# Kernel tuning notes

Hardware: AMD Instinct MI355X
Metric: run time of the kernel (lower is better)

The kernel has to match this reference:

```python
import jax, jax.numpy as jnp
import numpy as np

B, M, V, E, IN, OUT = 65536, 1_000_000, 2_000_000, 1_310_720, 64, 32
ALPHA = 0.2  # LeakyReLU negative slope (pyGAT default)


def setup_inputs() -> dict:
    key = jax.random.key(0)
    ks = jax.random.split(key, 11)
    return {
        "emb": jax.random.normal(ks[0], (V, IN), jnp.float32) * 0.1,
        "W_bal": jax.random.normal(ks[1], (IN, OUT), jnp.float32) * 0.1,
        "a_bal": jax.random.normal(ks[2], (2 * OUT,), jnp.float32) * 0.1,
        "W_unbal": jax.random.normal(ks[3], (IN, OUT), jnp.float32) * 0.1,
        "a_unbal": jax.random.normal(ks[4], (2 * OUT,), jnp.float32) * 0.1,
        "unique_ids": jax.random.randint(ks[5], (M,), 0, V, jnp.int32),
        "self_cols": jax.random.randint(ks[6], (B,), 0, M, jnp.int32),
        "pos_rows": jax.random.randint(ks[7], (E,), 0, B, jnp.int32),
        "pos_cols": jax.random.randint(ks[8], (E,), 0, M, jnp.int32),
        "neg_rows": jax.random.randint(ks[9], (E,), 0, B, jnp.int32),
        "neg_cols": jax.random.randint(ks[10], (E,), 0, M, jnp.int32),
    }


def _sp_gat(x, W, a, rows, cols, n_rows):
    # x: [M, IN] unique-node embeddings; rows: [Etot] in [0, n_rows); cols: [Etot] in [0, M)
    h = x @ W                                   # [M, OUT]
    src = h[rows]                               # [Etot, OUT] row-side features
    dst = h[cols]                               # [Etot, OUT] neighbor features
    score = jax.nn.leaky_relu(src @ a[:OUT] + dst @ a[OUT:], negative_slope=ALPHA)
    e = jnp.exp(-score)                         # [Etot] unnormalized attention
    denom = jax.ops.segment_sum(e, rows, num_segments=n_rows)            # [n_rows]
    num = jax.ops.segment_sum(e[:, None] * dst, rows, num_segments=n_rows)  # [n_rows, OUT]
    return jax.nn.elu(num / denom[:, None])


def reference(emb, W_bal, a_bal, W_unbal, a_unbal,
              unique_ids, self_cols, pos_rows, pos_cols, neg_rows, neg_cols):
    x = emb[unique_ids]                         # embedding lookup: [M, IN]
    self_rows = jnp.arange(B, dtype=jnp.int32)
    rows_p = jnp.concatenate([self_rows, pos_rows])
    cols_p = jnp.concatenate([self_cols, pos_cols])
    rows_n = jnp.concatenate([self_rows, neg_rows])
    cols_n = jnp.concatenate([self_cols, neg_cols])
    x_bal = _sp_gat(x, W_bal, a_bal, rows_p, cols_p, B)     # [B, OUT]
    x_unbal = _sp_gat(x, W_unbal, a_unbal, rows_n, cols_n, B)
    return (x_bal, x_unbal)
```

## Files before the change

### kernel.cpp

```cpp
#include <hip/hip_runtime.h>

#define B_N 65536
#define M_N 1000000
#define E_N 1310720
#define IN_D 64
#define OUT_D 32
#define BM 128
#define XS2 72
#define NCT 5
#define NFRAG (NCT * 2)
#define NBUCK 1024
#define BCAP 4096
#define BK_B 160

typedef __attribute__((ext_vector_type(8))) short bf16x8;
typedef __attribute__((ext_vector_type(4))) float f32x4;

__device__ __forceinline__ unsigned short f2bf(float f) {
  unsigned u = __float_as_uint(f);
  u += 0x7fffu + ((u >> 16) & 1u);
  return (unsigned short)(u >> 16);
}
__device__ __forceinline__ unsigned pk2(float a, float b) {
  return (unsigned)f2bf(a) | ((unsigned)f2bf(b) << 16);
}
__device__ __forceinline__ float bf2f(unsigned short s) {
  return __uint_as_float(((unsigned)s) << 16);
}

__global__ __launch_bounds__(256) void k_init(
    int* __restrict__ bucket_cnt,
    const float* __restrict__ Wb, const float* __restrict__ ab,
    const float* __restrict__ Wu, const float* __restrict__ au,
    unsigned* __restrict__ frag_buf)
{
  int t = threadIdx.x;
  if (blockIdx.x == 0) {
    ((int4*)bucket_cnt)[t] = (int4){0, 0, 0, 0};
    return;
  }
  for (int p = t; p < NFRAG * 64 * 4; p += 256) {
    int q = p >> 8;
    int rem = p & 255;
    int l = rem >> 2;
    int d = rem & 3;
    int ct = q >> 1, S = q & 1;
    int kb = 32 * S + 8 * (l >> 4);
    int n = 16 * ct + (l & 15);
    float v[2];
    #pragma unroll
    for (int e = 0; e < 2; ++e) {
      int kk = kb + 2 * d + e;
      float val;
      if (n < 32) val = Wb[kk * 32 + n];
      else if (n < 64) val = Wu[kk * 32 + (n - 32)];
      else if (n < 68) {
        const float* W = (n < 66) ? Wb : Wu;
        const float* av = (n < 66) ? ab : au;
        int hi = (n & 1) ? 32 : 0;
        float acc = 0.f;
        for (int j = 0; j < 32; ++j) acc = fmaf(W[kk * 32 + j], av[hi + j], acc);
        val = acc;
      } else val = 0.f;
      v[e] = val;
    }
    frag_buf[p] = pk2(v[0], v[1]);
  }
}

__global__ __launch_bounds__(1024) void k_bucket(
    const int* __restrict__ prow, const int* __restrict__ pcol,
    const int* __restrict__ nrow, const int* __restrict__ ncol,
    int* __restrict__ bucket_cnt, unsigned* __restrict__ bpack)
{
  __shared__ int hcnt[NBUCK];
  __shared__ int hbase[NBUCK];
  int t = threadIdx.x;
  int b = blockIdx.x;
  hcnt[t] = 0;
  __syncthreads();

  int br = (b >= 80) ? 1 : 0;
  const int* rows = br ? nrow : prow;
  const int* cols = br ? ncol : pcol;
  int ebase = (br ? (b - 80) : b) * 16384;

  int bins[16];
  int ranks[16];
  unsigned vals[16];
  #pragma unroll
  for (int j = 0; j < 16; ++j) {
    int i = ebase + j * 1024 + t;
    int r = rows[i];
    int c = cols[i];
    int bin = (br << 9) | (r >> 7);
    bins[j] = bin;
    vals[j] = ((unsigned)c << 7) | (unsigned)(r & 127);
    ranks[j] = atomicAdd(&hcnt[bin], 1);
  }
  __syncthreads();

  int cnt = hcnt[t];
  if (cnt > 0) hbase[t] = atomicAdd(&bucket_cnt[t], cnt);
  __syncthreads();

  #pragma unroll
  for (int j = 0; j < 16; ++j) {
    int bin = bins[j];
    int lpos = hbase[bin] + ranks[j];
    if (lpos < BCAP) bpack[(bin << 12) + lpos] = vals[j];
  }
}

__global__ __launch_bounds__(256) void k_hproj(
    const float* __restrict__ emb, const int* __restrict__ uids,
    const unsigned* __restrict__ frag_buf,
    unsigned short* __restrict__ hb, unsigned short* __restrict__ hu,
    float* __restrict__ adb, float* __restrict__ adu,
    float* __restrict__ asb, float* __restrict__ asu)
{
  __shared__ int suid[BM];
  __shared__ unsigned short sx[BM * XS2];
  int t = threadIdx.x;
  int nbase = blockIdx.x * BM;
  if (t < BM) suid[t] = (nbase + t < M_N) ? uids[nbase + t] : 0;
  __syncthreads();

  int chunk = t & 15, rb = t >> 4;
  #pragma unroll
  for (int i = 0; i < BM / 16; ++i) {
    int row = i * 16 + rb;
    float4 v = ((const float4*)emb)[(size_t)suid[row] * 16 + chunk];
    uint2 p;
    p.x = pk2(v.x, v.y);
    p.y = pk2(v.z, v.w);
    *(uint2*)&sx[row * XS2 + chunk * 4] = p;
  }
  __syncthreads();

  int l = t & 63, w = t >> 6;
  bf16x8 bf[NFRAG];
  #pragma unroll
  for (int q = 0; q < NFRAG; ++q)
    bf[q] = *(const bf16x8*)&frag_buf[(q * 64 + l) * 4];

  f32x4 acc[2][NCT];
  #pragma unroll
  for (int rt = 0; rt < 2; ++rt)
    #pragma unroll
    for (int ct = 0; ct < NCT; ++ct)
      acc[rt][ct] = (f32x4){0.f, 0.f, 0.f, 0.f};

  int wr0 = w * 32;
  #pragma unroll
  for (int rt = 0; rt < 2; ++rt) {
    const unsigned short* arow =
        &sx[(wr0 + rt * 16 + (l & 15)) * XS2 + (l >> 4) * 8];
    bf16x8 a0 = *(const bf16x8*)(arow);
    bf16x8 a1 = *(const bf16x8*)(arow + 32);
    #pragma unroll
    for (int ct = 0; ct < NCT; ++ct) {
      acc[rt][ct] = __builtin_amdgcn_mfma_f32_16x16x32_bf16(
          a0, bf[2 * ct + 0], acc[rt][ct], 0, 0, 0);
      acc[rt][ct] = __builtin_amdgcn_mfma_f32_16x16x32_bf16(
          a1, bf[2 * ct + 1], acc[rt][ct], 0, 0, 0);
    }
  }

  __syncthreads();
  unsigned short* sb = sx;
  unsigned short* su = sx + BM * 32;

  int g = l >> 4, cc = l & 15;
  #pragma unroll
  for (int rt = 0; rt < 2; ++rt) {
    int rl0 = wr0 + rt * 16 + g * 4;
    #pragma unroll
    for (int r = 0; r < 4; ++r) {
      int rl = rl0 + r;
      #pragma unroll
      for (int ct = 0; ct < 4; ++ct) {
        unsigned short hv = f2bf(acc[rt][ct][r]);
        if (ct < 2) sb[rl * 32 + ct * 16 + cc] = hv;
        else su[rl * 32 + (ct - 2) * 16 + cc] = hv;
      }
      int row = nbase + rl;
      if (row < M_N) {
        float dv = acc[rt][4][r];
        if (cc == 1) adb[row] = dv;
        else if (cc == 3) adu[row] = dv;
        else if (cc == 0) { if (row < B_N) asb[row] = dv; }
        else if (cc == 2) { if (row < B_N) asu[row] = dv; }
      }
    }
  }
  __syncthreads();

  const uint4* sb4 = (const uint4*)sb;
  const uint4* su4 = (const uint4*)su;
  uint4* hb4 = (uint4*)(hb + (size_t)nbase * 32);
  uint4* hu4 = (uint4*)(hu + (size_t)nbase * 32);
  int maxq = (M_N - nbase) * 4;
  #pragma unroll
  for (int k = 0; k < 2; ++k) {
    int idx = t + k * 256;
    if (idx < maxq) {
      hb4[idx] = sb4[idx];
      hu4[idx] = su4[idx];
    }
  }
}

__global__ __launch_bounds__(512) void k_agg2(
    const int* __restrict__ bucket_cnt, const unsigned* __restrict__ bpack,
    const int* __restrict__ selfc,
    const unsigned short* __restrict__ hb, const unsigned short* __restrict__ hu,
    const float* __restrict__ adb, const float* __restrict__ asb,
    const float* __restrict__ adu, const float* __restrict__ asu,
    float* __restrict__ out)
{
  __shared__ float asv[128];
  __shared__ int hist[128];
  __shared__ int sc[128];
  __shared__ int scol[BCAP];
  __shared__ float sev[BCAP];

  int t = threadIdx.x;
  int b = blockIdx.x;
  int br = b >> 9;
  int rbase = (b & 511) << 7;

  const unsigned short* h = br ? hu : hb;
  const float* adst = br ? adu : adb;
  const float* asrc = br ? asu : asb;

  if (t < 128) {
    hist[t] = 0;
    asv[t] = asrc[rbase + t];
  }
  __syncthreads();

  int cnt = bucket_cnt[b];
  if (cnt > BCAP) cnt = BCAP;
  const unsigned* bp = bpack + ((size_t)b << 12);

  unsigned v8[8];
  float ev8[8];
  int rk8[8];
  #pragma unroll
  for (int j = 0; j < 8; ++j) {
    int i = j * 512 + t;
    bool ok = i < cnt;
    unsigned v = ok ? bp[i] : 0u;
    int c = v >> 7;
    int r7 = v & 127;
    float s = asv[r7] + adst[c];
    float scv = s > 0.f ? s : 0.2f * s;
    v8[j] = v;
    ev8[j] = __expf(-scv);
    rk8[j] = ok ? atomicAdd(&hist[r7], 1) : 0;
  }
  __syncthreads();

  if (t < 128) sc[t] = hist[t];
  __syncthreads();
  for (int off = 1; off < 128; off <<= 1) {
    int add = (t < 128 && t >= off) ? sc[t - off] : 0;
    __syncthreads();
    if (t < 128) sc[t] += add;
    __syncthreads();
  }

  #pragma unroll
  for (int j = 0; j < 8; ++j) {
    int i = j * 512 + t;
    if (i < cnt) {
      unsigned v = v8[j];
      int r7 = v & 127;
      int pos = sc[r7] - hist[r7] + rk8[j];
      scol[pos] = v >> 7;
      sev[pos] = ev8[j];
    }
  }
  __syncthreads();

  int gid = t >> 5, lane = t & 31;
  for (int rr8 = 0; rr8 < 8; ++rr8) {
    int rr = gid * 8 + rr8;
    int r = rbase + rr;
    int s0 = sc[rr] - hist[rr];
    int n = hist[rr];

    int c0 = selfc[r];
    float sse = asv[rr] + adst[c0];
    float ssc = sse > 0.f ? sse : 0.2f * sse;
    float ev0 = __expf(-ssc);
    float acc = ev0 * bf2f(h[(size_t)c0 * 32 + lane]);
    float den = ev0;

    for (int j0 = 0; j0 < n; j0 += 8) {
      int c8[8];
      float e8[8];
      float hv8[8];
      #pragma unroll
      for (int q = 0; q < 8; ++q) {
        int j = j0 + q;
        int jj = (j < n) ? j : j0;
        c8[q] = scol[s0 + jj];
        e8[q] = (j < n) ? sev[s0 + jj] : 0.f;
      }
      #pragma unroll
      for (int q = 0; q < 8; ++q)
        hv8[q] = bf2f(h[(size_t)c8[q] * 32 + lane]);
      #pragma unroll
      for (int q = 0; q < 8; ++q) {
        acc = fmaf(e8[q], hv8[q], acc);
        den += e8[q];
      }
    }

    float x = acc / den;
    out[(((size_t)br * B_N + r) << 5) + lane] =
        (x > 0.f) ? x : (__expf(x) - 1.f);
  }
}

extern "C" void kernel_launch(void* const* d_in, const int* in_sizes, int n_in,
                              void* d_out, int out_size, void* d_ws, size_t ws_size,
                              hipStream_t stream) {
  const float* emb = (const float*)d_in[0];
  const float* Wb  = (const float*)d_in[1];
  const float* ab  = (const float*)d_in[2];
  const float* Wu  = (const float*)d_in[3];
  const float* au  = (const float*)d_in[4];
  const int* uids  = (const int*)d_in[5];
  const int* selfc = (const int*)d_in[6];
  const int* prow  = (const int*)d_in[7];
  const int* pcol  = (const int*)d_in[8];
  const int* nrow  = (const int*)d_in[9];
  const int* ncol  = (const int*)d_in[10];
  float* out = (float*)d_out;

  char* ws = (char*)d_ws;
  size_t off = 0;
  auto alloc = [&](size_t bytes) -> void* {
    void* p = ws + off;
    off += (bytes + 255) & ~(size_t)255;
    return p;
  };
  unsigned short* hb = (unsigned short*)alloc((size_t)M_N * OUT_D * 2);
  unsigned short* hu = (unsigned short*)alloc((size_t)M_N * OUT_D * 2);
  float* adb = (float*)alloc((size_t)M_N * 4);
  float* adu = (float*)alloc((size_t)M_N * 4);
  float* asb = (float*)alloc((size_t)B_N * 4);
  float* asu = (float*)alloc((size_t)B_N * 4);
  unsigned* frag_buf = (unsigned*)alloc((size_t)NFRAG * 64 * 4 * 4);
  int* bucket_cnt = (int*)alloc((size_t)NBUCK * 4);
  unsigned* bpack = (unsigned*)alloc((size_t)NBUCK * BCAP * 4);

  k_init<<<2, 256, 0, stream>>>(bucket_cnt, Wb, ab, Wu, au, frag_buf);

  k_bucket<<<BK_B, 1024, 0, stream>>>(prow, pcol, nrow, ncol,
                                      bucket_cnt, bpack);

  k_hproj<<<(M_N + BM - 1) / BM, 256, 0, stream>>>(emb, uids, frag_buf,
                                                   hb, hu, adb, adu, asb, asu);

  k_agg2<<<NBUCK, 512, 0, stream>>>(bucket_cnt, bpack, selfc,
                                    hb, hu, adb, asb, adu, asu, out);
}
```

Measured before the change: 185.9 us.

## Fuse edge bucketing and node projection into one interleaved kernel launch

Merges the edge-bucketing kernel and the embedding-projection kernel into a single launch. Every 13th block does bucketing on a smaller 4096-edge slice with 256 threads, and the remaining blocks do the projection. Interleaving lets the two independent stages overlap on the GPU and removes one launch and the gap between kernels. The cost is smaller bucket slices, which means more global atomics on the bucket counts, plus a shared-memory footprint sized to the larger of the two roles.

After: 201.1 us. 1.08x slower.

```diff
diff --git a/kernel.cpp b/kernel.cpp
--- a/kernel.cpp
+++ b/kernel.cpp
@@ -11,7 +11,8 @@
 #define NFRAG (NCT * 2)
 #define NBUCK 1024
 #define BCAP 4096
-#define BK_B 160
+#define BK2_B 640
+#define HP_B ((M_N + BM - 1) / BM)
 
 typedef __attribute__((ext_vector_type(8))) short bf16x8;
 typedef __attribute__((ext_vector_type(4))) float f32x4;
@@ -68,61 +69,74 @@
   }
 }
 
-__global__ __launch_bounds__(1024) void k_bucket(
+__global__ __launch_bounds__(256) void k_mid(
+    const float* __restrict__ emb, const int* __restrict__ uids,
+    const unsigned* __restrict__ frag_buf,
+    unsigned short* __restrict__ hb, unsigned short* __restrict__ hu,
+    float* __restrict__ adb, float* __restrict__ adu,
+    float* __restrict__ asb, float* __restrict__ asu,
     const int* __restrict__ prow, const int* __restrict__ pcol,
     const int* __restrict__ nrow, const int* __restrict__ ncol,
     int* __restrict__ bucket_cnt, unsigned* __restrict__ bpack)
 {
-  __shared__ int hcnt[NBUCK];
-  __shared__ int hbase[NBUCK];
+  __shared__ __align__(16) char smem[BM * XS2 * 2 + 512];
   int t = threadIdx.x;
   int b = blockIdx.x;
-  hcnt[t] = 0;
-  __syncthreads();
-
-  int br = (b >= 80) ? 1 : 0;
-  const int* rows = br ? nrow : prow;
-  const int* cols = br ? ncol : pcol;
-  int ebase = (br ? (b - 80) : b) * 16384;
-
-  int bins[16];
-  int ranks[16];
-  unsigned vals[16];
-  #pragma unroll
-  for (int j = 0; j < 16; ++j) {
-    int i = ebase + j * 1024 + t;
-    int r = rows[i];
-    int c = cols[i];
-    int bin = (br << 9) | (r >> 7);
-    bins[j] = bin;
-    vals[j] = ((unsigned)c << 7) | (unsigned)(r & 127);
-    ranks[j] = atomicAdd(&hcnt[bin], 1);
-  }
-  __syncthreads();
-
-  int cnt = hcnt[t];
-  if (cnt > 0) hbase[t] = atomicAdd(&bucket_cnt[t], cnt);
-  __syncthreads();
-
-  #pragma unroll
-  for (int j = 0; j < 16; ++j) {
-    int bin = bins[j];
-    int lpos = hbase[bin] + ranks[j];
-    if (lpos < BCAP) bpack[(bin << 12) + lpos] = vals[j];
-  }
-}
-
-__global__ __launch_bounds__(256) void k_hproj(
-    const float* __restrict__ emb, const int* __restrict__ uids,
-    const unsigned* __restrict__ frag_buf,
-    unsigned short* __restrict__ hb, unsigned short* __restrict__ hu,
-    float* __restrict__ adb, float* __restrict__ adu,
-    float* __restrict__ asb, float* __restrict__ asu)
-{
-  __shared__ int suid[BM];
-  __shared__ unsigned short sx[BM * XS2];
-  int t = threadIdx.x;
-  int nbase = blockIdx.x * BM;
+  int q13 = b / 13;
+  bool isb = ((b % 13) == 0) && (q13 < BK2_B);
+
+  if (isb) {
+    int* hcnt = (int*)smem;
+    int* hbase = hcnt + NBUCK;
+    ((int4*)hcnt)[t] = (int4){0, 0, 0, 0};
+    __syncthreads();
+
+    int s_id = q13;
+    int br = (s_id >= 320) ? 1 : 0;
+    const int* rows = br ? nrow : prow;
+    const int* cols = br ? ncol : pcol;
+    int ebase = (br ? (s_id - 320) : s_id) * 4096;
+
+    int bins[16];
+    int ranks[16];
+    unsigned vals[16];
+    #pragma unroll
+    for (int j = 0; j < 16; ++j) {
+      int i = ebase + j * 256 + t;
+      int r = rows[i];
+      int c = cols[i];
+      int bin = (br << 9) | (r >> 7);
+      bins[j] = bin;
+      vals[j] = ((unsigned)c << 7) | (unsigned)(r & 127);
+      ranks[j] = atomicAdd(&hcnt[bin], 1);
+    }
+    __syncthreads();
+
+    #pragma unroll
+    for (int k = 0; k < 4; ++k) {
+      int bin = k * 256 + t;
+      int cnt = hcnt[bin];
+      if (cnt > 0) hbase[bin] = atomicAdd(&bucket_cnt[bin], cnt);
+    }
+    __syncthreads();
+
+    #pragma unroll
+    for (int j = 0; j < 16; ++j) {
+      int bin = bins[j];
+      int lpos = hbase[bin] + ranks[j];
+      if (lpos < BCAP) bpack[(bin << 12) + lpos] = vals[j];
+    }
+    return;
+  }
+
+  int nbuck_before = ((b % 13) == 0) ? BK2_B
+                     : ((q13 + 1 < BK2_B) ? q13 + 1 : BK2_B);
+  int h_id = b - nbuck_before;
+
+  int* suid = (int*)smem;
+  unsigned short* sx = (unsigned short*)(smem + 512);
+
+  int nbase = h_id * BM;
   if (t < BM) suid[t] = (nbase + t < M_N) ? uids[nbase + t] : 0;
   __syncthreads();
 
@@ -360,11 +374,10 @@
 
   k_init<<<2, 256, 0, stream>>>(bucket_cnt, Wb, ab, Wu, au, frag_buf);
 
-  k_bucket<<<BK_B, 1024, 0, stream>>>(prow, pcol, nrow, ncol,
-                                      bucket_cnt, bpack);
-
-  k_hproj<<<(M_N + BM - 1) / BM, 256, 0, stream>>>(emb, uids, frag_buf,
-                                                   hb, hu, adb, adu, asb, asu);
+  k_mid<<<BK2_B + HP_B, 256, 0, stream>>>(emb, uids, frag_buf,
+                                          hb, hu, adb, adu, asb, asu,
+                                          prow, pcol, nrow, ncol,
+                                          bucket_cnt, bpack);
 
   k_agg2<<<NBUCK, 512, 0, stream>>>(bucket_cnt, bpack, selfc,
                                     hb, hu, adb, asb, adu, asu, out);
```
